# Performance work log

Measured on AMD Instinct MI355X. Metric: run time of the kernel, lower is better.

## Reference

```python
import jax, jax.numpy as jnp
import numpy as np

N_NODES = 100000
N_EDGES = 800000
F_IN, HID, N_CLS = 256, 128, 32


def setup_inputs() -> dict:
    key = jax.random.key(0)
    k1, k2, k3, k4, k5 = jax.random.split(key, 5)
    features = jax.random.normal(k1, (N_NODES, F_IN), dtype=jnp.float32)
    # random directed edges with no self loops (so add_remaining_self_loops == append all loops)
    src = jax.random.randint(k2, (N_EDGES,), 0, N_NODES)
    off = jax.random.randint(k3, (N_EDGES,), 1, N_NODES)
    dst = (src + off) % N_NODES
    edge_index = jnp.stack([src, dst]).astype(jnp.int64)
    # Glorot-style params for the two GCNConv layers
    W1 = jax.random.normal(k4, (F_IN, HID), dtype=jnp.float32) * (1.0 / np.sqrt(F_IN))
    b1 = jnp.zeros((HID,), dtype=jnp.float32)
    W2 = jax.random.normal(k5, (HID, N_CLS), dtype=jnp.float32) * (1.0 / np.sqrt(HID))
    b2 = jnp.zeros((N_CLS,), dtype=jnp.float32)
    return {"features": features, "edge_index": edge_index, "W1": W1, "b1": b1, "W2": W2, "b2": b2}


def _gcn_conv(x, W, b, src, dst, norm, n):
    xw = x @ W                                  # [N, d_out] dense GEMM
    msg = xw[src] * norm[:, None]               # gather + scale, [E, d_out]
    out = jax.ops.segment_sum(msg, dst, num_segments=n)  # scatter-add to targets
    return out + b


def reference(features, edge_index, W1, b1, W2, b2):
    n = features.shape[0]
    # add_remaining_self_loops (input has none, so append all)
    loops = jnp.arange(n, dtype=edge_index.dtype)
    src = jnp.concatenate([edge_index[0], loops])
    dst = jnp.concatenate([edge_index[1], loops])
    # gcn_norm: deg over targets, sym normalization deg^-1/2 A deg^-1/2
    deg = jax.ops.segment_sum(jnp.ones_like(src, dtype=features.dtype), dst, num_segments=n)
    dinv = jnp.where(deg > 0, jax.lax.rsqrt(deg), 0.0)
    norm = dinv[src] * dinv[dst]
    x = _gcn_conv(features, W1, b1, src, dst, norm, n)
    x = jax.nn.relu(x)
    # dropout is identity at inference (training=False)
    x = _gcn_conv(x, W2, b2, src, dst, norm, n)
    return jax.nn.log_softmax(x, axis=1)
```

## Files before the change

### kernel.cpp

```cpp
#include <hip/hip_runtime.h>
#include <hip/hip_bf16.h>

typedef __bf16 bf16_t;
typedef __attribute__((ext_vector_type(8))) __bf16 bf16x8;
typedef __attribute__((ext_vector_type(4))) float f32x4;

__global__ void k_deg_count(const int* __restrict__ dst, int* __restrict__ deg, int E) {
    int e = blockIdx.x * blockDim.x + threadIdx.x;
    if (e < E) atomicAdd(&deg[dst[e]], 1);
}

__global__ __launch_bounds__(256) void k_dinv_scan1(const int* __restrict__ deg,
                                                    float* __restrict__ dinv,
                                                    int* __restrict__ bsum, int n) {
    __shared__ int red[256];
    int b = blockIdx.x, t = threadIdx.x;
    int base = b * 1024 + t * 4;
    int s = 0;
#pragma unroll
    for (int j = 0; j < 4; ++j) {
        int i = base + j;
        if (i < n) { int d = deg[i]; s += d; dinv[i] = rsqrtf((float)(d + 1)); }
    }
    red[t] = s;
    __syncthreads();
    for (int d = 128; d > 0; d >>= 1) {
        if (t < d) red[t] += red[t + d];
        __syncthreads();
    }
    if (t == 0) bsum[b] = red[0];
}

__global__ __launch_bounds__(256) void k_scan2(int* __restrict__ bsum, int nb,
                                               int* __restrict__ rowPtr, int n) {
    __shared__ int s[256];
    int t = threadIdx.x;
    int v = (t < nb) ? bsum[t] : 0;
    s[t] = v;
    __syncthreads();
    for (int d = 1; d < 256; d <<= 1) {
        int u = (t >= d) ? s[t - d] : 0;
        __syncthreads();
        s[t] += u;
        __syncthreads();
    }
    if (t < nb) bsum[t] = s[t] - v;
    if (t == 255) rowPtr[n] = s[255];
}

__global__ __launch_bounds__(256) void k_scan3(const int* __restrict__ deg,
                                               const int* __restrict__ bsum,
                                               int* __restrict__ rowPtr, int n) {
    __shared__ int red[256];
    int b = blockIdx.x, t = threadIdx.x;
    int base = b * 1024 + t * 4;
    int v[4]; int s = 0;
#pragma unroll
    for (int j = 0; j < 4; ++j) { int i = base + j; v[j] = (i < n) ? deg[i] : 0; s += v[j]; }
    red[t] = s;
    __syncthreads();
    for (int d = 1; d < 256; d <<= 1) {
        int u = (t >= d) ? red[t - d] : 0;
        __syncthreads();
        red[t] += u;
        __syncthreads();
    }
    int run = bsum[b] + red[t] - s;
#pragma unroll
    for (int j = 0; j < 4; ++j) { int i = base + j; if (i < n) rowPtr[i] = run; run += v[j]; }
}

__global__ void k_scatter(const int* __restrict__ src, const int* __restrict__ dst,
                          const float* __restrict__ dinv, const int* __restrict__ rowPtr,
                          int* __restrict__ cursor, int2* __restrict__ edata, int E) {
    int e = blockIdx.x * blockDim.x + threadIdx.x;
    if (e >= E) return;
    int s = src[e], d = dst[e];
    int pos = rowPtr[d] + atomicAdd(&cursor[d], 1);
    int2 p; p.x = s; p.y = __float_as_int(dinv[s] * dinv[d]);
    edata[pos] = p;
}

__device__ inline void packB_one(const float* __restrict__ B, bf16_t* __restrict__ Bp,
                                 int N, int idx) {
    int j    = idx & 7;
    int lane = (idx >> 3) & 63;
    int st   = idx >> 9;
    int nt   = N >> 4;
    int s = st / nt, t = st - s * nt;
    int k = s * 32 + (lane >> 4) * 8 + j;
    int n = t * 16 + (lane & 15);
    Bp[idx] = (bf16_t)B[(size_t)k * N + n];
}

__global__ void k_packBoth(const float* __restrict__ W1, bf16_t* __restrict__ Bp1,
                           const float* __restrict__ W2, bf16_t* __restrict__ Bp2) {
    int idx = blockIdx.x * blockDim.x + threadIdx.x;
    const int T1 = (256 / 32) * (128 / 16) * 512;
    const int T2 = (128 / 32) * (32 / 16) * 512;
    if (idx < T1) packB_one(W1, Bp1, 128, idx);
    else if (idx < T1 + T2) packB_one(W2, Bp2, 32, idx - T1);
}

template <int KSTEPS, int NTILES>
__global__ __launch_bounds__(256) void k_gemm_pf32(
        const float* __restrict__ A, const bf16_t* __restrict__ Bp,
        bf16_t* __restrict__ C, int M) {
    int wave = (blockIdx.x * blockDim.x + threadIdx.x) >> 6;
    if (wave * 16 >= M) return;
    int lane = threadIdx.x & 63;
    int r16 = lane & 15, quad = lane >> 4;
    const int K = KSTEPS * 32, N = NTILES * 16;
    f32x4 acc[NTILES] = {};
    const float* arow = A + (size_t)(wave * 16 + r16) * K + quad * 8;
#pragma unroll
    for (int s = 0; s < KSTEPS; ++s) {
        const float* ap = arow + s * 32;
        bf16x8 a;
#pragma unroll
        for (int j = 0; j < 8; ++j) a[j] = (bf16_t)ap[j];
        const bf16_t* bp = Bp + ((size_t)(s * NTILES) * 64 + lane) * 8;
#pragma unroll
        for (int t = 0; t < NTILES; ++t) {
            bf16x8 b = *(const bf16x8*)(bp + t * 512);
            acc[t] = __builtin_amdgcn_mfma_f32_16x16x32_bf16(a, b, acc[t], 0, 0, 0);
        }
    }
#pragma unroll
    for (int t = 0; t < NTILES; ++t)
#pragma unroll
        for (int r = 0; r < 4; ++r)
            C[(size_t)(wave * 16 + quad * 4 + r) * N + t * 16 + r16] = (bf16_t)acc[t][r];
}

template <int KSTEPS, int NTILES>
__global__ __launch_bounds__(256) void k_gemm_pa16(
        const bf16_t* __restrict__ A, const bf16_t* __restrict__ Bp,
        bf16_t* __restrict__ C, int M) {
    int wave = (blockIdx.x * blockDim.x + threadIdx.x) >> 6;
    if (wave * 16 >= M) return;
    int lane = threadIdx.x & 63;
    int r16 = lane & 15, quad = lane >> 4;
    const int K = KSTEPS * 32, N = NTILES * 16;
    f32x4 acc[NTILES] = {};
    const bf16_t* arow = A + (size_t)(wave * 16 + r16) * K + quad * 8;
#pragma unroll
    for (int s = 0; s < KSTEPS; ++s) {
        bf16x8 a = *(const bf16x8*)(arow + s * 32);
        const bf16_t* bp = Bp + ((size_t)(s * NTILES) * 64 + lane) * 8;
#pragma unroll
        for (int t = 0; t < NTILES; ++t) {
            bf16x8 b = *(const bf16x8*)(bp + t * 512);
            acc[t] = __builtin_amdgcn_mfma_f32_16x16x32_bf16(a, b, acc[t], 0, 0, 0);
        }
    }
#pragma unroll
    for (int t = 0; t < NTILES; ++t)
#pragma unroll
        for (int r = 0; r < 4; ++r)
            C[(size_t)(wave * 16 + quad * 4 + r) * N + t * 16 + r16] = (bf16_t)acc[t][r];
}

__global__ __launch_bounds__(256) void k_agg1(
        const int* __restrict__ rowPtr, const int2* __restrict__ edata,
        const bf16_t* __restrict__ XW1, const float* __restrict__ dinv,
        const float* __restrict__ b1, bf16_t* __restrict__ H, int n) {
    int wave = (blockIdx.x * blockDim.x + threadIdx.x) >> 6;
    if (wave >= n) return;
    int lane = threadIdx.x & 63;
    int fl = (lane & 15) << 3;
    int h  = lane >> 4;
    int r0 = rowPtr[wave], r1 = rowPtr[wave + 1];
    float a0[8] = {}, a1[8] = {};
    int k = r0 + h;
    for (; k + 4 < r1; k += 8) {
        int2 e0 = edata[k], e1 = edata[k + 4];
        float w0 = __int_as_float(e0.y), w1 = __int_as_float(e1.y);
        bf16x8 x0 = *(const bf16x8*)(XW1 + ((size_t)e0.x << 7) + fl);
        bf16x8 x1 = *(const bf16x8*)(XW1 + ((size_t)e1.x << 7) + fl);
#pragma unroll
        for (int j = 0; j < 8; ++j) { a0[j] += (float)x0[j] * w0; a1[j] += (float)x1[j] * w1; }
    }
    if (k < r1) {
        int2 e0 = edata[k];
        float w0 = __int_as_float(e0.y);
        bf16x8 x0 = *(const bf16x8*)(XW1 + ((size_t)e0.x << 7) + fl);
#pragma unroll
        for (int j = 0; j < 8; ++j) a0[j] += (float)x0[j] * w0;
    }
#pragma unroll
    for (int j = 0; j < 8; ++j) {
        a0[j] += a1[j];
        a0[j] += __shfl_xor(a0[j], 16);
        a0[j] += __shfl_xor(a0[j], 32);
    }
    if (h == 0) {
        float d = dinv[wave], d2 = d * d;
        bf16x8 xs = *(const bf16x8*)(XW1 + ((size_t)wave << 7) + fl);
        bf16x8 hv;
#pragma unroll
        for (int j = 0; j < 8; ++j) {
            float v = a0[j] + (float)xs[j] * d2 + b1[fl + j];
            hv[j] = (bf16_t)fmaxf(v, 0.f);
        }
        *(bf16x8*)(H + ((size_t)wave << 7) + fl) = hv;
    }
}

__global__ __launch_bounds__(256) void k_agg2(
        const int* __restrict__ rowPtr, const int2* __restrict__ edata,
        const bf16_t* __restrict__ XW2, const float* __restrict__ dinv,
        const float* __restrict__ b2, float* __restrict__ out, int n) {
    int wave = (blockIdx.x * blockDim.x + threadIdx.x) >> 6;
    if (wave >= n) return;
    int lane = threadIdx.x & 63;
    int f = lane & 31, h = lane >> 5;
    int r0 = rowPtr[wave], r1 = rowPtr[wave + 1];
    float acc0 = 0.f, acc1 = 0.f;
    int k = r0 + h;
    for (; k + 2 < r1; k += 4) {
        int2 e0 = edata[k], e1 = edata[k + 2];
        acc0 += (float)XW2[((size_t)e0.x << 5) + f] * __int_as_float(e0.y);
        acc1 += (float)XW2[((size_t)e1.x << 5) + f] * __int_as_float(e1.y);
    }
    if (k < r1) {
        int2 e0 = edata[k];
        acc0 += (float)XW2[((size_t)e0.x << 5) + f] * __int_as_float(e0.y);
    }
    float acc = acc0 + acc1;
    acc += __shfl_xor(acc, 32);
    float d = dinv[wave];
    float v = acc + (float)XW2[((size_t)wave << 5) + f] * d * d + b2[f];
    float mx = v;
#pragma unroll
    for (int m = 16; m >= 1; m >>= 1) mx = fmaxf(mx, __shfl_xor(mx, m));
    float s = expf(v - mx);
#pragma unroll
    for (int m = 16; m >= 1; m >>= 1) s += __shfl_xor(s, m);
    if (lane < 32) out[((size_t)wave << 5) + f] = v - mx - logf(s);
}

extern "C" void kernel_launch(void* const* d_in, const int* in_sizes, int n_in,
                              void* d_out, int out_size, void* d_ws, size_t ws_size,
                              hipStream_t stream) {
    const float* feat = (const float*)d_in[0];
    const int*   eidx = (const int*)d_in[1];
    const float* W1   = (const float*)d_in[2];
    const float* b1   = (const float*)d_in[3];
    const float* W2   = (const float*)d_in[4];
    const float* b2   = (const float*)d_in[5];
    float* out = (float*)d_out;

    const int FIN = 256, HID = 128, NCLS = 32;
    const int N = in_sizes[0] / FIN;
    const int E = in_sizes[1] / 2;
    const int* src = eidx;
    const int* dst = eidx + E;

    char* ws = (char*)d_ws;
    size_t o = 0;
    auto alloc = [&](size_t bytes) -> void* {
        void* p = ws + o;
        o = (o + bytes + 255) & ~(size_t)255;
        return p;
    };
    int*    deg    = (int*)   alloc((size_t)N * 4);
    int*    cursor = (int*)   alloc((size_t)N * 4);
    size_t  zlen   = (size_t)((char*)(cursor + N) - (char*)deg);
    float*  dinv   = (float*) alloc((size_t)N * 4);
    int*    rowPtr = (int*)   alloc((size_t)(N + 1) * 4);
    int*    bsum   = (int*)   alloc(256 * 4);
    bf16_t* Bp1    = (bf16_t*)alloc((size_t)(FIN / 32) * (HID / 16) * 512 * 2);
    bf16_t* Bp2    = (bf16_t*)alloc((size_t)(HID / 32) * (NCLS / 16) * 512 * 2);
    int2*   edata  = (int2*)  alloc((size_t)E * 8);
    bf16_t* XW1    = (bf16_t*)alloc((size_t)N * HID * 2);
    bf16_t* H      = (bf16_t*)alloc((size_t)N * HID * 2);
    bf16_t* XW2    = XW1;

    const int T = 256;
    const int NB = (N + 1023) >> 10;
    hipMemsetAsync(deg, 0, zlen, stream);
    k_deg_count <<<(E + T - 1) / T, T, 0, stream>>>(dst, deg, E);
    k_dinv_scan1<<<NB, T, 0, stream>>>(deg, dinv, bsum, N);
    k_scan2     <<<1, T, 0, stream>>>(bsum, NB, rowPtr, N);
    k_scan3     <<<NB, T, 0, stream>>>(deg, bsum, rowPtr, N);
    k_scatter   <<<(E + T - 1) / T, T, 0, stream>>>(src, dst, dinv, rowPtr, cursor, edata, E);
    k_packBoth  <<<(32768 + 4096 + T - 1) / T, T, 0, stream>>>(W1, Bp1, W2, Bp2);

    {
        int waves = (N + 15) / 16;
        k_gemm_pf32<8, 8><<<(waves * 64 + T - 1) / T, T, 0, stream>>>(feat, Bp1, XW1, N);
    }
    k_agg1<<<(N * 64 + T - 1) / T, T, 0, stream>>>(rowPtr, edata, XW1, dinv, b1, H, N);

    {
        int waves = (N + 15) / 16;
        k_gemm_pa16<4, 2><<<(waves * 64 + T - 1) / T, T, 0, stream>>>(H, Bp2, XW2, N);
    }
    k_agg2<<<(N * 64 + T - 1) / T, T, 0, stream>>>(rowPtr, edata, XW2, dinv, b2, out, N);
}
```

Measured before the change: 368.2 us.

## Fuse preprocessing kernels, overlap edge scatter with GEMM, widen agg2 loads

Merges weight packing and degree counting into one launch with int4 loads of dst. Edge scattering now runs as extra blocks inside the first GEMM launch, so the memory-bound CSR build overlaps the compute-bound GEMM. The cursor is initialised to rowPtr in scan3, which drops one memset region and the rowPtr add in the scatter. The layer-2 aggregation is restructured so each lane loads two packed bf16 values and four edges are in flight per wave, with a float2 output store. Fewer launches and better overlap are traded for heterogeneous blocks that can hurt occupancy and load balance.

```diff
diff --git a/kernel.cpp b/kernel.cpp
--- a/kernel.cpp
+++ b/kernel.cpp
@@ -4,82 +4,6 @@
 typedef __bf16 bf16_t;
 typedef __attribute__((ext_vector_type(8))) __bf16 bf16x8;
 typedef __attribute__((ext_vector_type(4))) float f32x4;
-
-__global__ void k_deg_count(const int* __restrict__ dst, int* __restrict__ deg, int E) {
-    int e = blockIdx.x * blockDim.x + threadIdx.x;
-    if (e < E) atomicAdd(&deg[dst[e]], 1);
-}
-
-__global__ __launch_bounds__(256) void k_dinv_scan1(const int* __restrict__ deg,
-                                                    float* __restrict__ dinv,
-                                                    int* __restrict__ bsum, int n) {
-    __shared__ int red[256];
-    int b = blockIdx.x, t = threadIdx.x;
-    int base = b * 1024 + t * 4;
-    int s = 0;
-#pragma unroll
-    for (int j = 0; j < 4; ++j) {
-        int i = base + j;
-        if (i < n) { int d = deg[i]; s += d; dinv[i] = rsqrtf((float)(d + 1)); }
-    }
-    red[t] = s;
-    __syncthreads();
-    for (int d = 128; d > 0; d >>= 1) {
-        if (t < d) red[t] += red[t + d];
-        __syncthreads();
-    }
-    if (t == 0) bsum[b] = red[0];
-}
-
-__global__ __launch_bounds__(256) void k_scan2(int* __restrict__ bsum, int nb,
-                                               int* __restrict__ rowPtr, int n) {
-    __shared__ int s[256];
-    int t = threadIdx.x;
-    int v = (t < nb) ? bsum[t] : 0;
-    s[t] = v;
-    __syncthreads();
-    for (int d = 1; d < 256; d <<= 1) {
-        int u = (t >= d) ? s[t - d] : 0;
-        __syncthreads();
-        s[t] += u;
-        __syncthreads();
-    }
-    if (t < nb) bsum[t] = s[t] - v;
-    if (t == 255) rowPtr[n] = s[255];
-}
-
-__global__ __launch_bounds__(256) void k_scan3(const int* __restrict__ deg,
-                                               const int* __restrict__ bsum,
-                                               int* __restrict__ rowPtr, int n) {
-    __shared__ int red[256];
-    int b = blockIdx.x, t = threadIdx.x;
-    int base = b * 1024 + t * 4;
-    int v[4]; int s = 0;
-#pragma unroll
-    for (int j = 0; j < 4; ++j) { int i = base + j; v[j] = (i < n) ? deg[i] : 0; s += v[j]; }
-    red[t] = s;
-    __syncthreads();
-    for (int d = 1; d < 256; d <<= 1) {
-        int u = (t >= d) ? red[t - d] : 0;
-        __syncthreads();
-        red[t] += u;
-        __syncthreads();
-    }
-    int run = bsum[b] + red[t] - s;
-#pragma unroll
-    for (int j = 0; j < 4; ++j) { int i = base + j; if (i < n) rowPtr[i] = run; run += v[j]; }
-}
-
-__global__ void k_scatter(const int* __restrict__ src, const int* __restrict__ dst,
-                          const float* __restrict__ dinv, const int* __restrict__ rowPtr,
-                          int* __restrict__ cursor, int2* __restrict__ edata, int E) {
-    int e = blockIdx.x * blockDim.x + threadIdx.x;
-    if (e >= E) return;
-    int s = src[e], d = dst[e];
-    int pos = rowPtr[d] + atomicAdd(&cursor[d], 1);
-    int2 p; p.x = s; p.y = __float_as_int(dinv[s] * dinv[d]);
-    edata[pos] = p;
-}
 
 __device__ inline void packB_one(const float* __restrict__ B, bf16_t* __restrict__ Bp,
                                  int N, int idx) {
@@ -93,44 +17,136 @@
     Bp[idx] = (bf16_t)B[(size_t)k * N + n];
 }
 
-__global__ void k_packBoth(const float* __restrict__ W1, bf16_t* __restrict__ Bp1,
-                           const float* __restrict__ W2, bf16_t* __restrict__ Bp2) {
-    int idx = blockIdx.x * blockDim.x + threadIdx.x;
-    const int T1 = (256 / 32) * (128 / 16) * 512;
-    const int T2 = (128 / 32) * (32 / 16) * 512;
-    if (idx < T1) packB_one(W1, Bp1, 128, idx);
-    else if (idx < T1 + T2) packB_one(W2, Bp2, 32, idx - T1);
+__global__ __launch_bounds__(256) void k_front(
+        const float* __restrict__ W1, bf16_t* __restrict__ Bp1,
+        const float* __restrict__ W2, bf16_t* __restrict__ Bp2,
+        const int* __restrict__ dst, int* __restrict__ deg, int E) {
+    int b = blockIdx.x, t = threadIdx.x;
+    const int PACK_BLOCKS = (32768 + 4096) / 256;
+    if (b < PACK_BLOCKS) {
+        int idx = b * 256 + t;
+        if (idx < 32768) packB_one(W1, Bp1, 128, idx);
+        else             packB_one(W2, Bp2, 32, idx - 32768);
+        return;
+    }
+    int i = (b - PACK_BLOCKS) * 1024 + t * 4;
+    if (i + 4 <= E) {
+        int4 v = *(const int4*)(dst + i);
+        atomicAdd(&deg[v.x], 1); atomicAdd(&deg[v.y], 1);
+        atomicAdd(&deg[v.z], 1); atomicAdd(&deg[v.w], 1);
+    } else {
+#pragma unroll
+        for (int j = 0; j < 4; ++j)
+            if (i + j < E) atomicAdd(&deg[dst[i + j]], 1);
+    }
+}
+
+__global__ __launch_bounds__(256) void k_dinv_scan1(const int* __restrict__ deg,
+                                                    float* __restrict__ dinv,
+                                                    int* __restrict__ bsum, int n) {
+    __shared__ int red[256];
+    int b = blockIdx.x, t = threadIdx.x;
+    int base = b * 1024 + t * 4;
+    int s = 0;
+#pragma unroll
+    for (int j = 0; j < 4; ++j) {
+        int i = base + j;
+        if (i < n) { int d = deg[i]; s += d; dinv[i] = rsqrtf((float)(d + 1)); }
+    }
+    red[t] = s;
+    __syncthreads();
+    for (int d = 128; d > 0; d >>= 1) {
+        if (t < d) red[t] += red[t + d];
+        __syncthreads();
+    }
+    if (t == 0) bsum[b] = red[0];
+}
+
+__global__ __launch_bounds__(256) void k_scan2(int* __restrict__ bsum, int nb,
+                                               int* __restrict__ rowPtr, int n) {
+    __shared__ int s[256];
+    int t = threadIdx.x;
+    int v = (t < nb) ? bsum[t] : 0;
+    s[t] = v;
+    __syncthreads();
+    for (int d = 1; d < 256; d <<= 1) {
+        int u = (t >= d) ? s[t - d] : 0;
+        __syncthreads();
+        s[t] += u;
+        __syncthreads();
+    }
+    if (t < nb) bsum[t] = s[t] - v;
+    if (t == 255) rowPtr[n] = s[255];
+}
+
+__global__ __launch_bounds__(256) void k_scan3(const int* __restrict__ deg,
+                                               const int* __restrict__ bsum,
+                                               int* __restrict__ rowPtr,
+                                               int* __restrict__ cursor, int n) {
+    __shared__ int red[256];
+    int b = blockIdx.x, t = threadIdx.x;
+    int base = b * 1024 + t * 4;
+    int v[4]; int s = 0;
+#pragma unroll
+    for (int j = 0; j < 4; ++j) { int i = base + j; v[j] = (i < n) ? deg[i] : 0; s += v[j]; }
+    red[t] = s;
+    __syncthreads();
+    for (int d = 1; d < 256; d <<= 1) {
+        int u = (t >= d) ? red[t - d] : 0;
+        __syncthreads();
+        red[t] += u;
+        __syncthreads();
+    }
+    int run = bsum[b] + red[t] - s;
+#pragma unroll
+    for (int j = 0; j < 4; ++j) {
+        int i = base + j;
+        if (i < n) { rowPtr[i] = run; cursor[i] = run; run += v[j]; }
+    }
 }
 
 template <int KSTEPS, int NTILES>
-__global__ __launch_bounds__(256) void k_gemm_pf32(
+__global__ __launch_bounds__(256) void k_gemm_scatter(
         const float* __restrict__ A, const bf16_t* __restrict__ Bp,
-        bf16_t* __restrict__ C, int M) {
-    int wave = (blockIdx.x * blockDim.x + threadIdx.x) >> 6;
-    if (wave * 16 >= M) return;
-    int lane = threadIdx.x & 63;
-    int r16 = lane & 15, quad = lane >> 4;
-    const int K = KSTEPS * 32, N = NTILES * 16;
-    f32x4 acc[NTILES] = {};
-    const float* arow = A + (size_t)(wave * 16 + r16) * K + quad * 8;
-#pragma unroll
-    for (int s = 0; s < KSTEPS; ++s) {
-        const float* ap = arow + s * 32;
-        bf16x8 a;
-#pragma unroll
-        for (int j = 0; j < 8; ++j) a[j] = (bf16_t)ap[j];
-        const bf16_t* bp = Bp + ((size_t)(s * NTILES) * 64 + lane) * 8;
-#pragma unroll
-        for (int t = 0; t < NTILES; ++t) {
-            bf16x8 b = *(const bf16x8*)(bp + t * 512);
-            acc[t] = __builtin_amdgcn_mfma_f32_16x16x32_bf16(a, b, acc[t], 0, 0, 0);
+        bf16_t* __restrict__ C, int M, int gemmBlocks,
+        const int* __restrict__ src, const int* __restrict__ dst,
+        const float* __restrict__ dinv, int* __restrict__ cursor,
+        int2* __restrict__ edata, int E) {
+    int b = blockIdx.x, t = threadIdx.x;
+    if (b < gemmBlocks) {
+        int wave = (b * 256 + t) >> 6;
+        if (wave * 16 >= M) return;
+        int lane = t & 63;
+        int r16 = lane & 15, quad = lane >> 4;
+        const int K = KSTEPS * 32, N = NTILES * 16;
+        f32x4 acc[NTILES] = {};
+        const float* arow = A + (size_t)(wave * 16 + r16) * K + quad * 8;
+#pragma unroll
+        for (int s = 0; s < KSTEPS; ++s) {
+            const float* ap = arow + s * 32;
+            bf16x8 a;
+#pragma unroll
+            for (int j = 0; j < 8; ++j) a[j] = (bf16_t)ap[j];
+            const bf16_t* bp = Bp + ((size_t)(s * NTILES) * 64 + lane) * 8;
+#pragma unroll
+            for (int tt = 0; tt < NTILES; ++tt) {
+                bf16x8 bb = *(const bf16x8*)(bp + tt * 512);
+                acc[tt] = __builtin_amdgcn_mfma_f32_16x16x32_bf16(a, bb, acc[tt], 0, 0, 0);
+            }
         }
-    }
-#pragma unroll
-    for (int t = 0; t < NTILES; ++t)
-#pragma unroll
-        for (int r = 0; r < 4; ++r)
-            C[(size_t)(wave * 16 + quad * 4 + r) * N + t * 16 + r16] = (bf16_t)acc[t][r];
+#pragma unroll
+        for (int tt = 0; tt < NTILES; ++tt)
+#pragma unroll
+            for (int r = 0; r < 4; ++r)
+                C[(size_t)(wave * 16 + quad * 4 + r) * N + tt * 16 + r16] = (bf16_t)acc[tt][r];
+        return;
+    }
+    int e = (b - gemmBlocks) * 256 + t;
+    if (e >= E) return;
+    int s = src[e], d = dst[e];
+    int pos = atomicAdd(&cursor[d], 1);
+    int2 p; p.x = s; p.y = __float_as_int(dinv[s] * dinv[d]);
+    edata[pos] = p;
 }
 
 template <int KSTEPS, int NTILES>
@@ -214,30 +230,47 @@
     int wave = (blockIdx.x * blockDim.x + threadIdx.x) >> 6;
     if (wave >= n) return;
     int lane = threadIdx.x & 63;
-    int f = lane & 31, h = lane >> 5;
+    int g = lane & 15;
+    int h = lane >> 4;
     int r0 = rowPtr[wave], r1 = rowPtr[wave + 1];
-    float acc0 = 0.f, acc1 = 0.f;
+    float a00 = 0.f, a01 = 0.f, a10 = 0.f, a11 = 0.f;
     int k = r0 + h;
-    for (; k + 2 < r1; k += 4) {
-        int2 e0 = edata[k], e1 = edata[k + 2];
-        acc0 += (float)XW2[((size_t)e0.x << 5) + f] * __int_as_float(e0.y);
-        acc1 += (float)XW2[((size_t)e1.x << 5) + f] * __int_as_float(e1.y);
+    for (; k + 4 < r1; k += 8) {
+        int2 e0 = edata[k], e1 = edata[k + 4];
+        float w0 = __int_as_float(e0.y), w1 = __int_as_float(e1.y);
+        unsigned p0 = *(const unsigned*)(XW2 + ((size_t)e0.x << 5) + 2 * g);
+        unsigned p1 = *(const unsigned*)(XW2 + ((size_t)e1.x << 5) + 2 * g);
+        a00 += __int_as_float(p0 << 16) * w0;
+        a01 += __int_as_float(p0 & 0xffff0000u) * w0;
+        a10 += __int_as_float(p1 << 16) * w1;
+        a11 += __int_as_float(p1 & 0xffff0000u) * w1;
     }
     if (k < r1) {
         int2 e0 = edata[k];
-        acc0 += (float)XW2[((size_t)e0.x << 5) + f] * __int_as_float(e0.y);
-    }
-    float acc = acc0 + acc1;
-    acc += __shfl_xor(acc, 32);
-    float d = dinv[wave];
-    float v = acc + (float)XW2[((size_t)wave << 5) + f] * d * d + b2[f];
-    float mx = v;
-#pragma unroll
-    for (int m = 16; m >= 1; m >>= 1) mx = fmaxf(mx, __shfl_xor(mx, m));
-    float s = expf(v - mx);
-#pragma unroll
-    for (int m = 16; m >= 1; m >>= 1) s += __shfl_xor(s, m);
-    if (lane < 32) out[((size_t)wave << 5) + f] = v - mx - logf(s);
+        float w0 = __int_as_float(e0.y);
+        unsigned p0 = *(const unsigned*)(XW2 + ((size_t)e0.x << 5) + 2 * g);
+        a00 += __int_as_float(p0 << 16) * w0;
+        a01 += __int_as_float(p0 & 0xffff0000u) * w0;
+    }
+    float v0 = a00 + a10, v1 = a01 + a11;
+    v0 += __shfl_xor(v0, 16); v0 += __shfl_xor(v0, 32);
+    v1 += __shfl_xor(v1, 16); v1 += __shfl_xor(v1, 32);
+    float d = dinv[wave], d2 = d * d;
+    unsigned ps = *(const unsigned*)(XW2 + ((size_t)wave << 5) + 2 * g);
+    float2 bb = *(const float2*)(b2 + 2 * g);
+    v0 += __int_as_float(ps << 16) * d2 + bb.x;
+    v1 += __int_as_float(ps & 0xffff0000u) * d2 + bb.y;
+    float mx = fmaxf(v0, v1);
+#pragma unroll
+    for (int m = 8; m >= 1; m >>= 1) mx = fmaxf(mx, __shfl_xor(mx, m));
+    float s = expf(v0 - mx) + expf(v1 - mx);
+#pragma unroll
+    for (int m = 8; m >= 1; m >>= 1) s += __shfl_xor(s, m);
+    if (h == 0) {
+        float ls = logf(s);
+        float2 o; o.x = v0 - mx - ls; o.y = v1 - mx - ls;
+        *(float2*)(out + ((size_t)wave << 5) + 2 * g) = o;
+    }
 }
 
 extern "C" void kernel_launch(void* const* d_in, const int* in_sizes, int n_in,
@@ -266,7 +299,6 @@
     };
     int*    deg    = (int*)   alloc((size_t)N * 4);
     int*    cursor = (int*)   alloc((size_t)N * 4);
-    size_t  zlen   = (size_t)((char*)(cursor + N) - (char*)deg);
     float*  dinv   = (float*) alloc((size_t)N * 4);
     int*    rowPtr = (int*)   alloc((size_t)(N + 1) * 4);
     int*    bsum   = (int*)   alloc(256 * 4);
@@ -279,17 +311,20 @@
 
     const int T = 256;
     const int NB = (N + 1023) >> 10;
-    hipMemsetAsync(deg, 0, zlen, stream);
-    k_deg_count <<<(E + T - 1) / T, T, 0, stream>>>(dst, deg, E);
+    const int PACK_BLOCKS = (32768 + 4096) / 256;
+    const int DEG_BLOCKS  = (E + 1023) / 1024;
+    hipMemsetAsync(deg, 0, (size_t)N * 4, stream);
+    k_front     <<<PACK_BLOCKS + DEG_BLOCKS, T, 0, stream>>>(W1, Bp1, W2, Bp2, dst, deg, E);
     k_dinv_scan1<<<NB, T, 0, stream>>>(deg, dinv, bsum, N);
     k_scan2     <<<1, T, 0, stream>>>(bsum, NB, rowPtr, N);
-    k_scan3     <<<NB, T, 0, stream>>>(deg, bsum, rowPtr, N);
-    k_scatter   <<<(E + T - 1) / T, T, 0, stream>>>(src, dst, dinv, rowPtr, cursor, edata, E);
-    k_packBoth  <<<(32768 + 4096 + T - 1) / T, T, 0, stream>>>(W1, Bp1, W2, Bp2);
+    k_scan3     <<<NB, T, 0, stream>>>(deg, bsum, rowPtr, cursor, N);
 
     {
         int waves = (N + 15) / 16;
-        k_gemm_pf32<8, 8><<<(waves * 64 + T - 1) / T, T, 0, stream>>>(feat, Bp1, XW1, N);
+        int gemmBlocks = (waves * 64 + T - 1) / T;
+        int scatBlocks = (E + T - 1) / T;
+        k_gemm_scatter<8, 8><<<gemmBlocks + scatBlocks, T, 0, stream>>>(
+            feat, Bp1, XW1, N, gemmBlocks, src, dst, dinv, cursor, edata, E);
     }
     k_agg1<<<(N * 64 + T - 1) / T, T, 0, stream>>>(rowPtr, edata, XW1, dinv, b1, H, N);
 
```

After: 343.3 us. -6.8%, faster.
